# Optimization experiments

Hardware: AMD Instinct MI355X
Metric: run time of the kernel (lower is better)

The kernel has to match this reference:

```python
import jax, jax.numpy as jnp
import numpy as np

D_MODEL = 1024
NHEAD = 16
HEAD_DIM = D_MODEL // NHEAD


def setup_inputs() -> dict:
    key = jax.random.key(0)
    ks = jax.random.split(key, 9)
    B, T = 2, 2048
    s = 1.0 / np.sqrt(D_MODEL)
    return {
        "sequence": jax.random.normal(ks[0], (B, T, D_MODEL), dtype=jnp.float32),
        "wq": jax.random.normal(ks[1], (D_MODEL, D_MODEL), dtype=jnp.float32) * s,
        "bq": jax.random.normal(ks[2], (D_MODEL,), dtype=jnp.float32) * 0.01,
        "wk": jax.random.normal(ks[3], (D_MODEL, D_MODEL), dtype=jnp.float32) * s,
        "bk": jax.random.normal(ks[4], (D_MODEL,), dtype=jnp.float32) * 0.01,
        "wv": jax.random.normal(ks[5], (D_MODEL, D_MODEL), dtype=jnp.float32) * s,
        "bv": jax.random.normal(ks[6], (D_MODEL,), dtype=jnp.float32) * 0.01,
        "wo": jax.random.normal(ks[7], (D_MODEL, D_MODEL), dtype=jnp.float32) * s,
        "bo": jax.random.normal(ks[8], (D_MODEL,), dtype=jnp.float32) * 0.01,
    }


def reference(sequence, wq, bq, wk, bk, wv, bv, wo, bo):
    B, T, C = sequence.shape
    scale = jnp.asarray(HEAD_DIM ** 0.5, sequence.dtype)
    # projections (nn.Linear: x @ W.T + b)
    def proj(x, w, b):
        y = x @ w.T + b
        return y.reshape(B, T, NHEAD, HEAD_DIM).transpose(0, 2, 1, 3)  # [B,H,T,Dh]
    q = proj(sequence, wq, bq)
    k = proj(sequence, wk, bk)
    v = proj(sequence, wv, bv)
    scores = jnp.einsum("bhqd,bhkd->bhqk", q, k) / scale
    causal = jnp.tril(jnp.ones((T, T), dtype=bool))
    scores = jnp.where(causal, scores, jnp.asarray(-jnp.inf, scores.dtype))
    attn = jax.nn.softmax(scores, axis=-1)
    out = jnp.einsum("bhqk,bhkd->bhqd", attn, v)
    out = out.transpose(0, 2, 1, 3).reshape(B, T, C)
    return out @ wo.T + bo
```

## Files before the change

kernel.cpp:

```cpp
#include <hip/hip_runtime.h>
#include <hip/hip_bf16.h>
#include <hip/hip_fp16.h>
#include <type_traits>

#define DM 1024
#define NH 16
#define HD 64
#define BATCH 2
#define SEQ 2048
#define MROWS (BATCH*SEQ)

typedef __hip_bfloat16 bf16;
typedef __attribute__((ext_vector_type(8))) short    bf16x8;
typedef __attribute__((ext_vector_type(8))) short    s16x8;
typedef __attribute__((ext_vector_type(8))) _Float16 f16x8;
typedef __attribute__((ext_vector_type(4))) _Float16 f16x4;
typedef __attribute__((ext_vector_type(4))) short    s16x4;
typedef __attribute__((ext_vector_type(4))) float    f32x4;

#define LOG2E 1.44269504f
#define M_FIX 4.0f

__device__ __forceinline__ short f2bf(float x) {
    union { float f; unsigned u; } v; v.f = x;
    unsigned r = v.u + 0x7FFF + ((v.u >> 16) & 1);
    return (short)(r >> 16);
}

__device__ __forceinline__ bf16x8 ld8f(const float* p) {
    const float4 a = *(const float4*)p;
    const float4 b = *(const float4*)(p + 4);
    bf16x8 r;
    r[0]=f2bf(a.x); r[1]=f2bf(a.y); r[2]=f2bf(a.z); r[3]=f2bf(a.w);
    r[4]=f2bf(b.x); r[5]=f2bf(b.y); r[6]=f2bf(b.z); r[7]=f2bf(b.w);
    return r;
}

__device__ __forceinline__ void gload_lds16(const void* g, void* l) {
    __builtin_amdgcn_global_load_lds(
        (const __attribute__((address_space(1))) void*)g,
        (__attribute__((address_space(3))) void*)l, 16, 0, 0);
}

__global__ __launch_bounds__(256)
void cvt_bf16(const float* __restrict__ s0, const float* __restrict__ s1,
              const float* __restrict__ s2, const float* __restrict__ s3,
              const float* __restrict__ s4,
              short* d0, short* d1, short* d2, short* d3, short* d4)
{
    const int y = blockIdx.y;
    const float* src = (y==0? s0 : y==1? s1 : y==2? s2 : y==3? s3 : s4);
    short*       dst = (y==0? d0 : y==1? d1 : y==2? d2 : y==3? d3 : d4);
    const int n = (y == 0) ? MROWS*DM : DM*DM;
    const int i = (blockIdx.x * 256 + threadIdx.x) * 8;
    if (i < n) *(bf16x8*)(dst + i) = ld8f(src + i);
}

template<int MODE>
__device__ __forceinline__
void gemm_epilogue(f32x4 (&acc)[4][4], const float* bi, void* out, int z,
                   int tile_m, int tile_n, int wm, int wn,
                   int fr, int quad, int lane, short* lA)
{
    if (MODE == 1 && z == 2) {
        __syncthreads();
        short* sc = lA + (int)(threadIdx.x >> 6) * 256;
        const int rd = lane >> 2, tc = lane & 3;
        #pragma unroll
        for (int mi = 0; mi < 4; ++mi) {
            #pragma unroll
            for (int ni = 0; ni < 4; ++ni) {
                const int colg = tile_n + wn + ni*16 + fr;
                const float bia = bi[colg];
                f16x4 w;
                #pragma unroll
                for (int r = 0; r < 4; ++r) w[r] = (_Float16)(acc[mi][ni][r] + bia);
                *(f16x4*)(sc + fr*16 + quad*4) = w;
                const f16x4 vv = *(const f16x4*)(sc + rd*16 + tc*4);
                const int dg = tile_n + wn + ni*16 + rd;
                const int tg = tile_m + wm + mi*16 + tc*4;
                const int hh = dg >> 6, dd = dg & (HD-1);
                const int bb = tg >> 11, tt = tg & (SEQ-1);
                const int kt = tt >> 5, tko = tt & 31;
                *(f16x4*)((_Float16*)out +
                    ((((size_t)(bb*NH + hh))*(SEQ/32) + kt)*HD + dd)*32 + tko) = vv;
            }
        }
    } else {
        #pragma unroll
        for (int mi = 0; mi < 4; ++mi) {
            #pragma unroll
            for (int ni = 0; ni < 4; ++ni) {
                const int colg = tile_n + wn + ni*16 + fr;
                const float bia = bi[colg];
                #pragma unroll
                for (int r = 0; r < 4; ++r) {
                    const int rowg = tile_m + wm + mi*16 + quad*4 + r;
                    const float v = acc[mi][ni][r] + bia;
                    if (MODE == 0) {
                        ((float*)out)[(size_t)rowg*DM + colg] = v;
                    } else {
                        const int bb = rowg >> 11, t = rowg & (SEQ-1);
                        const int h  = colg >> 6,  d = colg & (HD-1);
                        ((_Float16*)out)[(((size_t)(bb*NH + h))*SEQ + t)*HD + d] = (_Float16)v;
                    }
                }
            }
        }
    }
}

template<int MODE>
__global__ __launch_bounds__(256)
void gemm_a(const short* __restrict__ A,
            const short* __restrict__ W0, const short* __restrict__ W1, const short* __restrict__ W2,
            const float* __restrict__ b0, const float* __restrict__ b1, const float* __restrict__ b2,
            void* o0, void* o1, void* o2)
{
    __shared__ __align__(16) short lA[128*32];
    __shared__ __align__(16) short lB[128*32];

    const int tid  = threadIdx.x;
    const int wid  = tid >> 6;
    const int lane = tid & 63;
    const int tile_n = blockIdx.x * 128;
    const int tile_m = blockIdx.y * 128;
    const int z = blockIdx.z;

    const short* Wg = (z == 0 ? W0 : (z == 1 ? W1 : W2));
    const float* bi = (z == 0 ? b0 : (z == 1 ? b1 : b2));
    void*        out = (z == 0 ? o0 : (z == 1 ? o1 : o2));

    const int sa_row = tile_m + wid*32 + (lane >> 2);
    const int sb_row = tile_n + wid*32 + (lane >> 2);
    const int scol   = (lane & 3) * 8;
    short* lA0 = lA + wid*1024 + lane*8;
    short* lA1 = lA0 + 512;
    short* lB0 = lB + wid*1024 + lane*8;
    short* lB1 = lB0 + 512;

    const int wm = (wid >> 1) * 64;
    const int wn = (wid & 1) * 64;
    const int fr = lane & 15;
    const int quad = lane >> 4;
    const int fq = quad * 8;

    f32x4 acc[4][4] = {};

    for (int k0 = 0; k0 < DM; k0 += 32) {
        __syncthreads();
        gload_lds16(A  + (size_t)sa_row*DM      + k0 + scol, lA0);
        gload_lds16(A  + (size_t)(sa_row+16)*DM + k0 + scol, lA1);
        gload_lds16(Wg + (size_t)sb_row*DM      + k0 + scol, lB0);
        gload_lds16(Wg + (size_t)(sb_row+16)*DM + k0 + scol, lB1);
        __syncthreads();

        bf16x8 af[4], bfv[4];
        #pragma unroll
        for (int i = 0; i < 4; ++i) af[i]  = *(const bf16x8*)(lA + (wm + i*16 + fr)*32 + fq);
        #pragma unroll
        for (int i = 0; i < 4; ++i) bfv[i] = *(const bf16x8*)(lB + (wn + i*16 + fr)*32 + fq);

        #pragma unroll
        for (int mi = 0; mi < 4; ++mi)
            #pragma unroll
            for (int ni = 0; ni < 4; ++ni)
                acc[mi][ni] = __builtin_amdgcn_mfma_f32_16x16x32_bf16(
                    af[mi], bfv[ni], acc[mi][ni], 0, 0, 0);
    }
    gemm_epilogue<MODE>(acc, bi, out, z, tile_m, tile_n, wm, wn, fr, quad, lane, lA);
}

template<typename TA, int MODE>
__global__ __launch_bounds__(256)
void gemm_f(const TA* __restrict__ A,
            const float* __restrict__ W0, const float* __restrict__ W1, const float* __restrict__ W2,
            const float* __restrict__ b0, const float* __restrict__ b1, const float* __restrict__ b2,
            void* o0, void* o1, void* o2)
{
    __shared__ __align__(16) short lA[128*32];
    __shared__ __align__(16) short lB[128*32];

    const int tid  = threadIdx.x;
    const int wid  = tid >> 6;
    const int lane = tid & 63;
    const int tile_n = blockIdx.x * 128;
    const int tile_m = blockIdx.y * 128;
    const int z = blockIdx.z;

    const float* Wg = (z == 0 ? W0 : (z == 1 ? W1 : W2));
    const float* bi = (z == 0 ? b0 : (z == 1 ? b1 : b2));
    void*        out = (z == 0 ? o0 : (z == 1 ? o1 : o2));

    const int sa_row = tile_m + wid*32 + (lane >> 2);
    const int sb_row = tile_n + wid*32 + (lane >> 2);
    const int scol   = (lane & 3) * 8;
    short* lA0 = lA + wid*1024 + lane*8;
    short* lA1 = lA0 + 512;
    short* lB0 = lB + wid*1024 + lane*8;
    short* lB1 = lB0 + 512;

    const int wm = (wid >> 1) * 64;
    const int wn = (wid & 1) * 64;
    const int fr = lane & 15;
    const int quad = lane >> 4;
    const int fq = quad * 8;

    f32x4 acc[4][4] = {};

    for (int k0 = 0; k0 < DM; k0 += 32) {
        bf16x8 ra0, ra1;
        if constexpr (std::is_same<TA, float>::value) {
            ra0 = ld8f((const float*)A + (size_t)sa_row*DM      + k0 + scol);
            ra1 = ld8f((const float*)A + (size_t)(sa_row+16)*DM + k0 + scol);
        } else {
            ra0 = *(const bf16x8*)((const short*)A + (size_t)sa_row*DM      + k0 + scol);
            ra1 = *(const bf16x8*)((const short*)A + (size_t)(sa_row+16)*DM + k0 + scol);
        }
        const bf16x8 rb0 = ld8f(Wg + (size_t)sb_row*DM      + k0 + scol);
        const bf16x8 rb1 = ld8f(Wg + (size_t)(sb_row+16)*DM + k0 + scol);

        __syncthreads();
        *(bf16x8*)lA0 = ra0;
        *(bf16x8*)lA1 = ra1;
        *(bf16x8*)lB0 = rb0;
        *(bf16x8*)lB1 = rb1;
        __syncthreads();

        bf16x8 af[4], bfv[4];
        #pragma unroll
        for (int i = 0; i < 4; ++i) af[i]  = *(const bf16x8*)(lA + (wm + i*16 + fr)*32 + fq);
        #pragma unroll
        for (int i = 0; i < 4; ++i) bfv[i] = *(const bf16x8*)(lB + (wn + i*16 + fr)*32 + fq);

        #pragma unroll
        for (int mi = 0; mi < 4; ++mi)
            #pragma unroll
            for (int ni = 0; ni < 4; ++ni)
                acc[mi][ni] = __builtin_amdgcn_mfma_f32_16x16x32_bf16(
                    af[mi], bfv[ni], acc[mi][ni], 0, 0, 0);
    }
    gemm_epilogue<MODE>(acc, bi, out, z, tile_m, tile_n, wm, wn, fr, quad, lane, lA);
}

__global__ __launch_bounds__(256)
void attn(const _Float16* __restrict__ Q, const _Float16* __restrict__ K,
          const _Float16* __restrict__ Vt, short* __restrict__ O)
{
    __shared__ __align__(16) _Float16 lsK[2048];
    __shared__ __align__(16) _Float16 lsV[2048];

    const int t    = threadIdx.x;
    const int lane = t & 63;
    const int wid  = t >> 6;
    const int id   = blockIdx.x;
    const int bh   = id & 31;
    const int xb   = id >> 5;
    const size_t base = (size_t)bh * SEQ * HD;
    const int qr = lane & 15;
    const int quad = lane >> 4;
    const int bb = bh >> 4, h = bh & (NH-1);

    const int k_goff = ((t>>2)&31)*64 + (t>>7)*32 + (t&3)*8;
    const int v_goff = (t&63)*32 + (t>>6)*8;
    _Float16* lsKp = lsK + t*8;
    _Float16* lsVp = lsV + t*8;

    const float SC1 = 0.125f * LOG2E;
    const float SC2 = -M_FIX * LOG2E;
    const int vboff = (quad>>1)*512 + (quad&1)*4 + qr*8;

    #pragma unroll 1
    for (int half = 0; half < 2; ++half) {
        const int band = half ? (31 - xb) : xb;
        const int q_tile = band*64 + wid*16;
        const int q_idx  = q_tile + qr;
        const int ntiles = 2*band + 2;
        const int ktm    = 2*band + (wid >> 1);

        const f16x8* Qv = (const f16x8*)(Q + base + (size_t)(q_tile + qr)*HD);
        const f16x8 qf0 = Qv[quad];
        const f16x8 qf1 = Qv[quad + 4];

        float l_cur = 0.f;
        f32x4 o[4] = {};

        #pragma unroll 1
        for (int kt = 0; kt < ntiles; ++kt) {
            __syncthreads();
            gload_lds16(K  + base + (size_t)kt*2048 + k_goff, lsKp);
            gload_lds16(Vt + base + (size_t)kt*2048 + v_goff, lsVp);
            __syncthreads();
            if (kt > ktm) continue;

            const f16x8 ka0 = *(const f16x8*)(lsK + qr*32 + quad*8);
            const f16x8 ka1 = *(const f16x8*)(lsK + 1024 + qr*32 + quad*8);
            const f16x8 kb0 = *(const f16x8*)(lsK + (16+qr)*32 + quad*8);
            const f16x8 kb1 = *(const f16x8*)(lsK + 1024 + (16+qr)*32 + quad*8);

            f32x4 s0 = {}, s1 = {};
            s0 = __builtin_amdgcn_mfma_f32_16x16x32_f16(ka0, qf0, s0, 0, 0, 0);
            s0 = __builtin_amdgcn_mfma_f32_16x16x32_f16(ka1, qf1, s0, 0, 0, 0);
            s1 = __builtin_amdgcn_mfma_f32_16x16x32_f16(kb0, qf0, s1, 0, 0, 0);
            s1 = __builtin_amdgcn_mfma_f32_16x16x32_f16(kb1, qf1, s1, 0, 0, 0);

            f16x4 p0, p1;
            const int k_base = kt*32;
            if (kt == ktm) {
                #pragma unroll
                for (int r = 0; r < 4; ++r) {
                    const int key = k_base + quad*4 + r;
                    float e0 = exp2f(s0[r] * SC1 + SC2);
                    float e1 = exp2f(s1[r] * SC1 + SC2);
                    e0 = (key      <= q_idx) ? e0 : 0.f;
                    e1 = (key + 16 <= q_idx) ? e1 : 0.f;
                    l_cur += e0 + e1;
                    p0[r] = (_Float16)e0;
                    p1[r] = (_Float16)e1;
                }
            } else {
                #pragma unroll
                for (int r = 0; r < 4; ++r) {
                    const float e0 = exp2f(s0[r] * SC1 + SC2);
                    const float e1 = exp2f(s1[r] * SC1 + SC2);
                    l_cur += e0 + e1;
                    p0[r] = (_Float16)e0;
                    p1[r] = (_Float16)e1;
                }
            }

            #pragma unroll
            for (int dt = 0; dt < 4; ++dt) {
                const f16x4 av0 = *(const f16x4*)(lsV + vboff + dt*128);
                const f16x4 av1 = *(const f16x4*)(lsV + 1024 + vboff + dt*128);
                o[dt] = __builtin_amdgcn_mfma_f32_16x16x16f16(av0, p0, o[dt], 0, 0, 0);
                o[dt] = __builtin_amdgcn_mfma_f32_16x16x16f16(av1, p1, o[dt], 0, 0, 0);
            }
        }

        l_cur += __shfl_xor(l_cur, 16, 64);
        l_cur += __shfl_xor(l_cur, 32, 64);
        const float linv = 1.0f / fmaxf(l_cur, 1e-30f);

        const int tq = q_tile + qr;
        #pragma unroll
        for (int dt = 0; dt < 4; ++dt) {
            s16x4 pk;
            #pragma unroll
            for (int r = 0; r < 4; ++r) pk[r] = f2bf(o[dt][r] * linv);
            *(s16x4*)(O + ((size_t)(bb*SEQ + tq))*DM + h*HD + dt*16 + quad*4) = pk;
        }
    }
}

extern "C" void kernel_launch(void* const* d_in, const int* in_sizes, int n_in,
                              void* d_out, int out_size, void* d_ws, size_t ws_size,
                              hipStream_t stream)
{
    const float* seq = (const float*)d_in[0];
    const float* wq  = (const float*)d_in[1];
    const float* bq  = (const float*)d_in[2];
    const float* wk  = (const float*)d_in[3];
    const float* bk  = (const float*)d_in[4];
    const float* wv  = (const float*)d_in[5];
    const float* bv  = (const float*)d_in[6];
    const float* wo  = (const float*)d_in[7];
    const float* bo  = (const float*)d_in[8];

    _Float16* Qb = (_Float16*)d_ws;
    _Float16* Kb = Qb + (size_t)MROWS*DM;
    _Float16* Vt = Kb + (size_t)MROWS*DM;
    short*    Ob = (short*)(Vt + (size_t)MROWS*DM);
    short*    sq16 = Ob + (size_t)MROWS*DM;
    short*    wq16 = sq16 + (size_t)MROWS*DM;
    short*    wk16 = wq16 + (size_t)DM*DM;
    short*    wv16 = wk16 + (size_t)DM*DM;
    short*    wo16 = wv16 + (size_t)DM*DM;

    const size_t need = ((size_t)MROWS*DM*2)*5 + ((size_t)DM*DM*2)*4;
    const bool fast = ws_size >= need;

    if (fast) {
        dim3 gc(MROWS*DM/(256*8), 5, 1);
        cvt_bf16<<<gc, 256, 0, stream>>>(seq, wq, wk, wv, wo,
                                         sq16, wq16, wk16, wv16, wo16);

        dim3 g1(DM/128, MROWS/128, 3);
        gemm_a<1><<<g1, 256, 0, stream>>>(sq16, wq16, wk16, wv16, bq, bk, bv,
                                          (void*)Qb, (void*)Kb, (void*)Vt);

        attn<<<dim3(512), 256, 0, stream>>>(Qb, Kb, Vt, Ob);

        dim3 g3(DM/128, MROWS/128, 1);
        gemm_a<0><<<g3, 256, 0, stream>>>(Ob, wo16, wo16, wo16, bo, bo, bo,
                                          d_out, d_out, d_out);
    } else {
        dim3 g1(DM/128, MROWS/128, 3);
        gemm_f<float, 1><<<g1, 256, 0, stream>>>(seq, wq, wk, wv, bq, bk, bv,
                                                 (void*)Qb, (void*)Kb, (void*)Vt);

        attn<<<dim3(512), 256, 0, stream>>>(Qb, Kb, Vt, Ob);

        dim3 g3(DM/128, MROWS/128, 1);
        gemm_f<short, 0><<<g3, 256, 0, stream>>>(Ob, wo, wo, wo, bo, bo, bo,
                                                 d_out, d_out, d_out);
    }
}
```

Baseline: 201.8 us.

## Double-buffer attention K/V loads, split bands per block, vectorize GEMM epilogue stores

The attention kernel now launches one block per query band instead of pairing two bands per block, and double-buffers K tiles in LDS. The next V tile is prefetched into registers and written into a padded LDS layout after compute, so global loads overlap the MFMA work. The GEMM epilogues for Q/K projection and the output projection now stage accumulators through LDS to emit 16-byte vector stores instead of scalar ones. The cost is more LDS use, an extra barrier per tile, and load imbalance because causal bands have very different lengths.

```diff
diff --git a/kernel.cpp b/kernel.cpp
--- a/kernel.cpp
+++ b/kernel.cpp
@@ -62,9 +62,10 @@
                    int tile_m, int tile_n, int wm, int wn,
                    int fr, int quad, int lane, short* lA)
 {
+    const int wid = (int)(threadIdx.x >> 6);
     if (MODE == 1 && z == 2) {
         __syncthreads();
-        short* sc = lA + (int)(threadIdx.x >> 6) * 256;
+        short* sc = lA + wid * 256;
         const int rd = lane >> 2, tc = lane & 3;
         #pragma unroll
         for (int mi = 0; mi < 4; ++mi) {
@@ -86,7 +87,35 @@
                     ((((size_t)(bb*NH + hh))*(SEQ/32) + kt)*HD + dd)*32 + tko) = vv;
             }
         }
+    } else if (MODE == 1) {
+        __syncthreads();
+        _Float16* sc = (_Float16*)lA + wid * 640;
+        const int tl = lane >> 2, qc = lane & 3;
+        #pragma unroll
+        for (int mi = 0; mi < 4; ++mi) {
+            #pragma unroll
+            for (int nip = 0; nip < 2; ++nip) {
+                #pragma unroll
+                for (int nn = 0; nn < 2; ++nn) {
+                    const int ni = nip*2 + nn;
+                    const int colg = tile_n + wn + ni*16 + fr;
+                    const float bia = bi[colg];
+                    #pragma unroll
+                    for (int r = 0; r < 4; ++r)
+                        sc[(quad*4 + r)*40 + nn*16 + fr] = (_Float16)(acc[mi][ni][r] + bia);
+                }
+                const f16x8 v = *(const f16x8*)(sc + tl*40 + qc*8);
+                const int d0 = tile_n + wn + nip*32 + qc*8;
+                const int hh = d0 >> 6, dd = d0 & (HD-1);
+                const int tg = tile_m + wm + mi*16 + tl;
+                const int bb = tg >> 11, tt = tg & (SEQ-1);
+                *(f16x8*)((_Float16*)out + (((size_t)(bb*NH + hh))*SEQ + tt)*HD + dd) = v;
+            }
+        }
     } else {
+        __syncthreads();
+        float* scf = (float*)lA + wid * 320;
+        const int tl = lane >> 2, qc = lane & 3;
         #pragma unroll
         for (int mi = 0; mi < 4; ++mi) {
             #pragma unroll
@@ -94,17 +123,12 @@
                 const int colg = tile_n + wn + ni*16 + fr;
                 const float bia = bi[colg];
                 #pragma unroll
-                for (int r = 0; r < 4; ++r) {
-                    const int rowg = tile_m + wm + mi*16 + quad*4 + r;
-                    const float v = acc[mi][ni][r] + bia;
-                    if (MODE == 0) {
-                        ((float*)out)[(size_t)rowg*DM + colg] = v;
-                    } else {
-                        const int bb = rowg >> 11, t = rowg & (SEQ-1);
-                        const int h  = colg >> 6,  d = colg & (HD-1);
-                        ((_Float16*)out)[(((size_t)(bb*NH + h))*SEQ + t)*HD + d] = (_Float16)v;
-                    }
-                }
+                for (int r = 0; r < 4; ++r)
+                    scf[(quad*4 + r)*20 + fr] = acc[mi][ni][r] + bia;
+                const float4 v = *(const float4*)(scf + tl*20 + qc*4);
+                const int rowg = tile_m + wm + mi*16 + tl;
+                const int c0 = tile_n + wn + ni*16 + qc*4;
+                *(float4*)((float*)out + (size_t)rowg*DM + c0) = v;
             }
         }
     }
@@ -247,56 +271,57 @@
 void attn(const _Float16* __restrict__ Q, const _Float16* __restrict__ K,
           const _Float16* __restrict__ Vt, short* __restrict__ O)
 {
-    __shared__ __align__(16) _Float16 lsK[2048];
-    __shared__ __align__(16) _Float16 lsV[2048];
+    __shared__ __align__(16) _Float16 lsK[2][2048];
+    __shared__ __align__(16) _Float16 lsV[64*40];
 
     const int t    = threadIdx.x;
     const int lane = t & 63;
     const int wid  = t >> 6;
     const int id   = blockIdx.x;
     const int bh   = id & 31;
-    const int xb   = id >> 5;
+    const int band = id >> 5;
     const size_t base = (size_t)bh * SEQ * HD;
     const int qr = lane & 15;
     const int quad = lane >> 4;
     const int bb = bh >> 4, h = bh & (NH-1);
 
+    const int q_tile = band*64 + wid*16;
+    const int q_idx  = q_tile + qr;
+    const int ntiles = 2*band + 2;
+    const int ktm    = 2*band + (wid >> 1);
+
     const int k_goff = ((t>>2)&31)*64 + (t>>7)*32 + (t&3)*8;
-    const int v_goff = (t&63)*32 + (t>>6)*8;
-    _Float16* lsKp = lsK + t*8;
-    _Float16* lsVp = lsV + t*8;
+    _Float16* vwr = lsV + (t>>2)*40 + (t&3)*8;
+
+    const f16x8* Qv = (const f16x8*)(Q + base + (size_t)(q_tile + qr)*HD);
+    const f16x8 qf0 = Qv[quad];
+    const f16x8 qf1 = Qv[quad + 4];
 
     const float SC1 = 0.125f * LOG2E;
     const float SC2 = -M_FIX * LOG2E;
-    const int vboff = (quad>>1)*512 + (quad&1)*4 + qr*8;
+
+    float l_cur = 0.f;
+    f32x4 o[4] = {};
+
+    gload_lds16(K + base + k_goff, lsK[0] + t*8);
+    f16x8 vreg = *(const f16x8*)(Vt + base + (size_t)t*8);
+    *(f16x8*)vwr = vreg;
 
     #pragma unroll 1
-    for (int half = 0; half < 2; ++half) {
-        const int band = half ? (31 - xb) : xb;
-        const int q_tile = band*64 + wid*16;
-        const int q_idx  = q_tile + qr;
-        const int ntiles = 2*band + 2;
-        const int ktm    = 2*band + (wid >> 1);
-
-        const f16x8* Qv = (const f16x8*)(Q + base + (size_t)(q_tile + qr)*HD);
-        const f16x8 qf0 = Qv[quad];
-        const f16x8 qf1 = Qv[quad + 4];
-
-        float l_cur = 0.f;
-        f32x4 o[4] = {};
-
-        #pragma unroll 1
-        for (int kt = 0; kt < ntiles; ++kt) {
-            __syncthreads();
-            gload_lds16(K  + base + (size_t)kt*2048 + k_goff, lsKp);
-            gload_lds16(Vt + base + (size_t)kt*2048 + v_goff, lsVp);
-            __syncthreads();
-            if (kt > ktm) continue;
-
-            const f16x8 ka0 = *(const f16x8*)(lsK + qr*32 + quad*8);
-            const f16x8 ka1 = *(const f16x8*)(lsK + 1024 + qr*32 + quad*8);
-            const f16x8 kb0 = *(const f16x8*)(lsK + (16+qr)*32 + quad*8);
-            const f16x8 kb1 = *(const f16x8*)(lsK + 1024 + (16+qr)*32 + quad*8);
+    for (int kt = 0; kt < ntiles; ++kt) {
+        const int cur = kt & 1;
+        __syncthreads();
+        if (kt + 1 < ntiles) {
+            gload_lds16(K + base + (size_t)(kt+1)*2048 + k_goff, lsK[1-cur] + t*8);
+            vreg = *(const f16x8*)(Vt + base + (size_t)(kt+1)*2048 + t*8);
+        }
+
+        if (kt <= ktm) {
+            const _Float16* lk = lsK[cur];
+            const f16x8 ka0 = *(const f16x8*)(lk + qr*32 + quad*8);
+            const f16x8 ka1 = *(const f16x8*)(lk + 1024 + qr*32 + quad*8);
+            const f16x8 kb0 = *(const f16x8*)(lk + (16+qr)*32 + quad*8);
+            const f16x8 kb1 = *(const f16x8*)(lk + 1024 + (16+qr)*32 + quad*8);
 
             f32x4 s0 = {}, s1 = {};
             s0 = __builtin_amdgcn_mfma_f32_16x16x32_f16(ka0, qf0, s0, 0, 0, 0);
@@ -331,25 +356,29 @@
 
             #pragma unroll
             for (int dt = 0; dt < 4; ++dt) {
-                const f16x4 av0 = *(const f16x4*)(lsV + vboff + dt*128);
-                const f16x4 av1 = *(const f16x4*)(lsV + 1024 + vboff + dt*128);
+                const _Float16* lv = lsV + (dt*16 + qr)*40 + quad*4;
+                const f16x4 av0 = *(const f16x4*)lv;
+                const f16x4 av1 = *(const f16x4*)(lv + 16);
                 o[dt] = __builtin_amdgcn_mfma_f32_16x16x16f16(av0, p0, o[dt], 0, 0, 0);
                 o[dt] = __builtin_amdgcn_mfma_f32_16x16x16f16(av1, p1, o[dt], 0, 0, 0);
             }
         }
 
-        l_cur += __shfl_xor(l_cur, 16, 64);
-        l_cur += __shfl_xor(l_cur, 32, 64);
-        const float linv = 1.0f / fmaxf(l_cur, 1e-30f);
-
-        const int tq = q_tile + qr;
-        #pragma unroll
-        for (int dt = 0; dt < 4; ++dt) {
-            s16x4 pk;
-            #pragma unroll
-            for (int r = 0; r < 4; ++r) pk[r] = f2bf(o[dt][r] * linv);
-            *(s16x4*)(O + ((size_t)(bb*SEQ + tq))*DM + h*HD + dt*16 + quad*4) = pk;
-        }
+        __syncthreads();
+        if (kt + 1 < ntiles) *(f16x8*)vwr = vreg;
+    }
+
+    l_cur += __shfl_xor(l_cur, 16, 64);
+    l_cur += __shfl_xor(l_cur, 32, 64);
+    const float linv = 1.0f / fmaxf(l_cur, 1e-30f);
+
+    const int tq = q_tile + qr;
+    #pragma unroll
+    for (int dt = 0; dt < 4; ++dt) {
+        s16x4 pk;
+        #pragma unroll
+        for (int r = 0; r < 4; ++r) pk[r] = f2bf(o[dt][r] * linv);
+        *(s16x4*)(O + ((size_t)(bb*SEQ + tq))*DM + h*HD + dt*16 + quad*4) = pk;
     }
 }
 
@@ -389,7 +418,7 @@
         gemm_a<1><<<g1, 256, 0, stream>>>(sq16, wq16, wk16, wv16, bq, bk, bv,
                                           (void*)Qb, (void*)Kb, (void*)Vt);
 
-        attn<<<dim3(512), 256, 0, stream>>>(Qb, Kb, Vt, Ob);
+        attn<<<dim3(1024), 256, 0, stream>>>(Qb, Kb, Vt, Ob);
 
         dim3 g3(DM/128, MROWS/128, 1);
         gemm_a<0><<<g3, 256, 0, stream>>>(Ob, wo16, wo16, wo16, bo, bo, bo,
@@ -399,7 +428,7 @@
         gemm_f<float, 1><<<g1, 256, 0, stream>>>(seq, wq, wk, wv, bq, bk, bv,
                                                  (void*)Qb, (void*)Kb, (void*)Vt);
 
-        attn<<<dim3(512), 256, 0, stream>>>(Qb, Kb, Vt, Ob);
+        attn<<<dim3(1024), 256, 0, stream>>>(Qb, Kb, Vt, Ob);
 
         dim3 g3(DM/128, MROWS/128, 1);
         gemm_f<short, 0><<<g3, 256, 0, stream>>>(Ob, wo, wo, wo, bo, bo, bo,
```

Result: slower. 207.1 us (+2.6%).
